# Kernel optimization log

Measured on AMD Instinct MI355X. Metric: run time of the kernel, lower is better.

The kernel has to match this reference:

```python
import jax, jax.numpy as jnp
import numpy as np

EMBED_DIM = 1024
N_HEADS = 16
HEAD_DIM = EMBED_DIM // N_HEADS


def setup_inputs() -> dict:
    key = jax.random.key(0)
    k_x, k_qw, k_qb, k_ow, k_ob = jax.random.split(key, 5)
    s = 1.0 / np.sqrt(EMBED_DIM)
    return {
        "x": jax.random.normal(k_x, (2, 2048, EMBED_DIM), dtype=jnp.float32),
        "qkv_w": jax.random.uniform(k_qw, (3 * EMBED_DIM, EMBED_DIM), jnp.float32, -s, s),
        "qkv_b": jax.random.uniform(k_qb, (3 * EMBED_DIM,), jnp.float32, -s, s),
        "out_w": jax.random.uniform(k_ow, (EMBED_DIM, EMBED_DIM), jnp.float32, -s, s),
        "out_b": jax.random.uniform(k_ob, (EMBED_DIM,), jnp.float32, -s, s),
    }


def reference(x, qkv_w, qkv_b, out_w, out_b):
    B, S, E = x.shape
    # fused QKV projection (torch Linear: x @ W^T + b)
    qkv = x @ qkv_w.T + qkv_b                      # [B,S,3E]
    qkv = qkv.reshape(B, S, N_HEADS, 3 * HEAD_DIM).transpose(0, 2, 1, 3)  # [B,H,S,3d]
    q, k, v = jnp.split(qkv, 3, axis=-1)           # each [B,H,S,d]
    scores = jnp.einsum("bhqd,bhkd->bhqk", q, k) / jnp.sqrt(jnp.float32(HEAD_DIM))
    weights = jax.nn.softmax(scores, axis=-1)      # [B,H,S,S]
    attn = jnp.einsum("bhqk,bhkd->bhqd", weights, v)
    attn = attn.transpose(0, 2, 1, 3).reshape(B, S, E)
    return attn @ out_w.T + out_b
```

## Files before the change

kernel.cpp:

```cpp
#include <hip/hip_runtime.h>
#include <hip/hip_bf16.h>


#define E_DIM   1024
#define NHEADS  16
#define HDIM    64
#define SEQ     2048
#define TOK     4096
#define QKV_DIM 3072
#define QK_STRIDE 2048
#define QSCALE_F 0.18033688011112042f

typedef __attribute__((ext_vector_type(8))) short bf16x8;
typedef __attribute__((ext_vector_type(4))) float f32x4;
typedef __attribute__((ext_vector_type(4))) int   i32x4;
typedef __attribute__((ext_vector_type(2))) int   i32x2;
typedef __attribute__((ext_vector_type(2))) __bf16 bf16x2_t;

#if __has_builtin(__builtin_amdgcn_exp2f)
#define EXP2F(x) __builtin_amdgcn_exp2f(x)
#else
#define EXP2F(x) exp2f(x)
#endif

__device__ __forceinline__ unsigned pack2bf(float a, float b) {
#if __has_builtin(__builtin_amdgcn_cvt_pk_bf16_f32)
    union { bf16x2_t v; unsigned u; } u;
    u.v = __builtin_amdgcn_cvt_pk_bf16_f32(a, b);
    return u.u;
#else
    union { float f; unsigned u; } ua, ub; ua.f = a; ub.f = b;
    unsigned ra = ua.u + 0x7FFF + ((ua.u >> 16) & 1);
    unsigned rb = ub.u + 0x7FFF + ((ub.u >> 16) & 1);
    return (ra >> 16) | (rb & 0xFFFF0000u);
#endif
}

__device__ __forceinline__ unsigned short f2bf(float x) {
    return (unsigned short)(pack2bf(x, x) & 0xFFFFu);
}

__device__ __forceinline__ void load_lds16(const void* g, void* l) {
    __builtin_amdgcn_global_load_lds(
        (const __attribute__((address_space(1))) void*)g,
        (__attribute__((address_space(3))) void*)l, 16, 0, 0);
}

__device__ __forceinline__ bf16x8 lds_read8(const unsigned short* p) {
    union { i32x4 i; bf16x8 b; } u;
    u.i = *(const i32x4*)p;
    return u.b;
}

__device__ __forceinline__ f32x4 mfma16(bf16x8 a, bf16x8 b, f32x4 c) {
    return __builtin_amdgcn_mfma_f32_16x16x32_bf16(a, b, c, 0, 0, 0);
}

__global__ void cast3_kernel(const float* __restrict__ a, unsigned short* __restrict__ oa, int na4,
                             const float* __restrict__ b, unsigned short* __restrict__ ob, int nb4,
                             const float* __restrict__ c, unsigned short* __restrict__ oc) {
    int i = blockIdx.x * blockDim.x + threadIdx.x;
    const float* src; unsigned short* dst; int j;
    if (i < na4)            { src = a; dst = oa; j = i; }
    else if (i < na4 + nb4) { src = b; dst = ob; j = i - na4; }
    else                    { src = c; dst = oc; j = i - na4 - nb4; }
    f32x4 v = ((const f32x4*)src)[j];
    union { i32x2 i2; unsigned u[2]; } o;
    o.u[0] = pack2bf(v.x, v.y);
    o.u[1] = pack2bf(v.z, v.w);
    ((i32x2*)dst)[j] = o.i2;
}

__global__ __launch_bounds__(256, 3)
void gemm_qkv_kernel(const unsigned short* __restrict__ A,
                     const unsigned short* __restrict__ B,
                     const float* __restrict__ bias,
                     unsigned short* __restrict__ qk,
                     unsigned short* __restrict__ vT,
                     int K) {
    __shared__ __align__(16) unsigned short As[128 * 64];
    __shared__ __align__(16) unsigned short Bs[128 * 64];

    const int tid  = threadIdx.x;
    const int wave = tid >> 6, lane = tid & 63;
    const int quad = lane >> 4, l16 = lane & 15;
    const int flat = blockIdx.y * 24 + blockIdx.x;
    const int xcd = flat & 7, idx = flat >> 3;
    const int row_blk = (xcd >> 1) * 8 + idx / 12;
    const int col_blk = (xcd & 1) * 12 + idx % 12;
    const int row0 = row_blk * 128, col0 = col_blk * 128;
    const int wr = (wave >> 1) * 64, wc = (wave & 1) * 64;

    f32x4 acc[4][4];
#pragma unroll
    for (int i = 0; i < 4; ++i)
#pragma unroll
        for (int j = 0; j < 4; ++j) acc[i][j] = (f32x4){0.f, 0.f, 0.f, 0.f};

    const int nkt = K >> 6;
    for (int kt = 0; kt < nkt; ++kt) {
        const int k0 = kt << 6;
#pragma unroll
        for (int i = 0; i < 4; ++i) {
            int p = i * 256 + tid;
            int r = p >> 3;
            int kc = (p & 7) ^ (r & 7);
            load_lds16(A + (size_t)(row0 + r) * K + k0 + kc * 8, &As[p * 8]);
        }
#pragma unroll
        for (int i = 0; i < 4; ++i) {
            int p = i * 256 + tid;
            int r = p >> 3;
            int kc = (p & 7) ^ (r & 7);
            load_lds16(B + (size_t)(col0 + r) * K + k0 + kc * 8, &Bs[p * 8]);
        }
        __syncthreads();

#pragma unroll
        for (int ks = 0; ks < 2; ++ks) {
            bf16x8 af[4], bfr[4];
#pragma unroll
            for (int rb = 0; rb < 4; ++rb) {
                int r_l  = wr + rb * 16 + l16;
                int phys = (ks * 4 + quad) ^ (l16 & 7);
                af[rb] = lds_read8(&As[r_l * 64 + phys * 8]);
            }
#pragma unroll
            for (int cb = 0; cb < 4; ++cb) {
                int r_l  = wc + cb * 16 + l16;
                int phys = (ks * 4 + quad) ^ (l16 & 7);
                bfr[cb] = lds_read8(&Bs[r_l * 64 + phys * 8]);
            }
#pragma unroll
            for (int rb = 0; rb < 4; ++rb)
#pragma unroll
                for (int cb = 0; cb < 4; ++cb)
                    acc[rb][cb] = mfma16(af[rb], bfr[cb], acc[rb][cb]);
        }
        __syncthreads();
    }

#pragma unroll
    for (int rb = 0; rb < 4; ++rb)
#pragma unroll
        for (int cb = 0; cb < 4; ++cb) {
            int col = col0 + wc + cb * 16 + l16;
            int h    = col / 192;
            int part = col - h * 192;
            float bv = bias[col];
            int row_b = row0 + wr + rb * 16 + quad * 4;
            float v[4];
#pragma unroll
            for (int reg = 0; reg < 4; ++reg) v[reg] = acc[rb][cb][reg] + bv;
            if (part < 128) {
                float sc = (part < 64) ? QSCALE_F : 1.0f;
                size_t base = (size_t)h * 128 + part;
#pragma unroll
                for (int reg = 0; reg < 4; ++reg)
                    qk[(size_t)(row_b + reg) * QK_STRIDE + base] = f2bf(v[reg] * sc);
            } else {
                int i  = part - 128;
                int b  = row_b >> 11;
                int s0 = row_b & 2047;
                int kk = s0 & 127;
                int cc = kk >> 4, qq = (kk >> 2) & 3;
                int sp = (s0 & ~127) | ((cc >> 1) << 5) | (qq << 3) | ((cc & 1) << 2);
                i32x2 pk;
                pk.x = (int)pack2bf(v[0], v[1]);
                pk.y = (int)pack2bf(v[2], v[3]);
                *(i32x2*)&vT[(((size_t)(b * 16 + h)) * 64 + i) * SEQ + sp] = pk;
            }
        }
}

__global__ __launch_bounds__(256, 2)
void gemm2_kernel(const unsigned short* __restrict__ A,
                  const unsigned short* __restrict__ B,
                  const float* __restrict__ bias,
                  float* __restrict__ C, int M, int N, int K) {
    __shared__ __align__(16) unsigned short As[128 * 64];
    __shared__ __align__(16) unsigned short Bs[64 * 64];

    const int tid  = threadIdx.x;
    const int wave = tid >> 6, lane = tid & 63;
    const int quad = lane >> 4, l16 = lane & 15;
    const int flat = blockIdx.y * 16 + blockIdx.x;
    const int xcd = flat & 7, idx = flat >> 3;
    const int row_blk = (xcd >> 1) * 8 + (idx >> 3);
    const int col_blk = (xcd & 1) * 8 + (idx & 7);
    const int row0 = row_blk * 128, col0 = col_blk * 64;
    const int wr = wave * 32;

    f32x4 acc[2][4];
#pragma unroll
    for (int i = 0; i < 2; ++i)
#pragma unroll
        for (int j = 0; j < 4; ++j) acc[i][j] = (f32x4){0.f, 0.f, 0.f, 0.f};

    const int nkt = K >> 6;
    for (int kt = 0; kt < nkt; ++kt) {
        const int k0 = kt << 6;
#pragma unroll
        for (int i = 0; i < 4; ++i) {
            int p = i * 256 + tid;
            int r = p >> 3;
            int kc = (p & 7) ^ (r & 7);
            load_lds16(A + (size_t)(row0 + r) * K + k0 + kc * 8, &As[p * 8]);
        }
#pragma unroll
        for (int i = 0; i < 2; ++i) {
            int p = i * 256 + tid;
            int r = p >> 3;
            int kc = (p & 7) ^ (r & 7);
            load_lds16(B + (size_t)(col0 + r) * K + k0 + kc * 8, &Bs[p * 8]);
        }
        __syncthreads();

#pragma unroll
        for (int ks = 0; ks < 2; ++ks) {
            bf16x8 af[2], bfr[4];
#pragma unroll
            for (int rb = 0; rb < 2; ++rb) {
                int r_l  = wr + rb * 16 + l16;
                int phys = (ks * 4 + quad) ^ (l16 & 7);
                af[rb] = lds_read8(&As[r_l * 64 + phys * 8]);
            }
#pragma unroll
            for (int cb = 0; cb < 4; ++cb) {
                int r_l  = cb * 16 + l16;
                int phys = (ks * 4 + quad) ^ (l16 & 7);
                bfr[cb] = lds_read8(&Bs[r_l * 64 + phys * 8]);
            }
#pragma unroll
            for (int rb = 0; rb < 2; ++rb)
#pragma unroll
                for (int cb = 0; cb < 4; ++cb)
                    acc[rb][cb] = mfma16(af[rb], bfr[cb], acc[rb][cb]);
        }
        __syncthreads();
    }

#pragma unroll
    for (int rb = 0; rb < 2; ++rb)
#pragma unroll
        for (int cb = 0; cb < 4; ++cb) {
            int col = col0 + cb * 16 + l16;
            float bv = bias[col];
#pragma unroll
            for (int reg = 0; reg < 4; ++reg) {
                int row = row0 + wr + rb * 16 + quad * 4 + reg;
                C[(size_t)row * N + col] = acc[rb][cb][reg] + bv;
            }
        }
}


#define STAGE_KV(BUF) do {                                                     \
    load_lds16(kg[0], lk[0] + (BUF) * 8192); kg[0] += 128 * QK_STRIDE;         \
    load_lds16(kg[1], lk[1] + (BUF) * 8192); kg[1] += 128 * QK_STRIDE;         \
    load_lds16(vg[0], lv[0] + (BUF) * 8192); vg[0] += 128;                     \
    load_lds16(vg[1], lv[1] + (BUF) * 8192); vg[1] += 128;                     \
} while (0)

#define COMPUTE_TILE(BUF) do {                                                 \
    constexpr int KO_ = (BUF) * 8192;                                          \
    f32x4 s[8];                                                                \
    _Pragma("unroll") for (int cb = 0; cb < 8; ++cb)                           \
        s[cb] = (f32x4){0.f, 0.f, 0.f, 0.f};                                   \
    __builtin_amdgcn_s_setprio(1);                                             \
    _Pragma("unroll") for (int cb = 0; cb < 8; ++cb) {                         \
        bf16x8 kf0 = lds_read8(Kb0 + KO_ + cb * 1024);                         \
        s[cb] = mfma16(kf0, qf[0], s[cb]);                                     \
    }                                                                          \
    _Pragma("unroll") for (int cb = 0; cb < 8; ++cb) {                         \
        bf16x8 kf1 = lds_read8(Kb1 + KO_ + cb * 1024);                         \
        s[cb] = mfma16(kf1, qf[1], s[cb]);                                     \
    }                                                                          \
    __builtin_amdgcn_s_setprio(0);                                             \
    _Pragma("unroll") for (int cb = 0; cb < 8; ++cb)                           \
        _Pragma("unroll") for (int r = 0; r < 4; ++r)                          \
            s[cb][r] = EXP2F(s[cb][r]);                                        \
    {                                                                          \
        f32x4 t0 = s[0] + s[1], t1 = s[2] + s[3];                              \
        f32x4 t2 = s[4] + s[5], t3 = s[6] + s[7];                              \
        t0 += t1; t2 += t3;                                                    \
        lsum += t0 + t2;                                                       \
    }                                                                          \
    __builtin_amdgcn_s_setprio(1);                                             \
    _Pragma("unroll") for (int ks2 = 0; ks2 < 4; ++ks2) {                      \
        union { i32x4 i; bf16x8 b; } pu;                                       \
        pu.i.x = (int)pack2bf(s[2 * ks2][0], s[2 * ks2][1]);                   \
        pu.i.y = (int)pack2bf(s[2 * ks2][2], s[2 * ks2][3]);                   \
        pu.i.z = (int)pack2bf(s[2 * ks2 + 1][0], s[2 * ks2 + 1][1]);           \
        pu.i.w = (int)pack2bf(s[2 * ks2 + 1][2], s[2 * ks2 + 1][3]);           \
        bf16x8 pf = pu.b;                                                      \
        _Pragma("unroll") for (int ib = 0; ib < 4; ++ib) {                     \
            bf16x8 vf = lds_read8(Vb[ks2] + KO_ + ib * 2048);                  \
            o[ib] = mfma16(pf, vf, o[ib]);                                     \
        }                                                                      \
    }                                                                          \
    __builtin_amdgcn_s_setprio(0);                                             \
} while (0)

__global__ __launch_bounds__(512, 4)
void attn_kernel(const unsigned short* __restrict__ qk,
                 const unsigned short* __restrict__ vT,
                 unsigned short* __restrict__ attn) {
    __shared__ __align__(16) unsigned short Ks[2][128 * 64];
    __shared__ __align__(16) unsigned short Vs[2][64 * 128];

    const int tid  = threadIdx.x;
    const int wave = tid >> 6, lane = tid & 63;
    const int quad = lane >> 4, l16 = lane & 15;

    const int flat = blockIdx.y * 16 + blockIdx.x;
    const int swz  = (flat & 7) * 64 + (flat >> 3);
    const int bh = swz >> 4;
    const int b = bh >> 4, h = bh & 15;
    const int q0 = (swz & 15) * 128;
    const size_t rowbase = (size_t)b * SEQ;
    const int qtok = q0 + wave * 16 + l16;

    const int sw3 = l16 & 7;
    const unsigned short* Kb0 = &Ks[0][l16 * 64 + ((quad ^ sw3) * 8)];
    const unsigned short* Kb1 = &Ks[0][l16 * 64 + (((4 + quad) ^ sw3) * 8)];
    const unsigned short* Vb[4] = {
        &Vs[0][l16 * 128 + (((0 * 4 + quad) ^ l16) * 8)],
        &Vs[0][l16 * 128 + (((1 * 4 + quad) ^ l16) * 8)],
        &Vs[0][l16 * 128 + (((2 * 4 + quad) ^ l16) * 8)],
        &Vs[0][l16 * 128 + (((3 * 4 + quad) ^ l16) * 8)] };

    const unsigned short* kg[2]; unsigned short* lk[2];
    const unsigned short* vg[2]; unsigned short* lv[2];
#pragma unroll
    for (int i = 0; i < 2; ++i) {
        int p = i * 512 + tid;
        { int r = p >> 3; int kc = (p & 7) ^ (r & 7);
          kg[i] = qk + (rowbase) * QK_STRIDE + h * 128 + 64 + (size_t)r * QK_STRIDE + kc * 8;
          lk[i] = &Ks[0][p * 8]; }
        { int r = p >> 4; int c = (p & 15) ^ (r & 15);
          vg[i] = vT + (size_t)bh * 64 * SEQ + (size_t)r * SEQ + c * 8;
          lv[i] = &Vs[0][p * 8]; }
    }

    bf16x8 qf[2];
#pragma unroll
    for (int ks = 0; ks < 2; ++ks) {
        const unsigned short* p =
            qk + (rowbase + qtok) * QK_STRIDE + h * 128 + ks * 32 + quad * 8;
        union { i32x4 i; bf16x8 b; } u;
        u.i = *(const i32x4*)p;
        qf[ks] = u.b;
    }

    f32x4 o[4];
#pragma unroll
    for (int ib = 0; ib < 4; ++ib) o[ib] = (f32x4){0.f, 0.f, 0.f, 0.f};
    f32x4 lsum = (f32x4){0.f, 0.f, 0.f, 0.f};

    STAGE_KV(0);
#pragma unroll 1
    for (int kt = 0; kt < SEQ / 128; kt += 2) {
        STAGE_KV(1);
        __asm__ volatile("s_waitcnt vmcnt(4)" ::: "memory");
        __builtin_amdgcn_s_barrier();
        COMPUTE_TILE(0);
        __builtin_amdgcn_s_barrier();
        if (kt + 2 < SEQ / 128) {
            STAGE_KV(0);
            __asm__ volatile("s_waitcnt vmcnt(4)" ::: "memory");
        } else {
            __asm__ volatile("s_waitcnt vmcnt(0)" ::: "memory");
        }
        __builtin_amdgcn_s_barrier();
        COMPUTE_TILE(1);
        __builtin_amdgcn_s_barrier();
    }

    float l_p = (lsum[0] + lsum[1]) + (lsum[2] + lsum[3]);
    l_p += __shfl_xor(l_p, 16);
    l_p += __shfl_xor(l_p, 32);

    float il[4];
#pragma unroll
    for (int r = 0; r < 4; ++r) il[r] = 1.0f / __shfl(l_p, quad * 4 + r);
#pragma unroll
    for (int ib = 0; ib < 4; ++ib)
#pragma unroll
        for (int r = 0; r < 4; ++r) {
            int t = q0 + wave * 16 + quad * 4 + r;
            attn[(rowbase + t) * E_DIM + h * 64 + ib * 16 + l16] =
                f2bf(o[ib][r] * il[r]);
        }
}

extern "C" void kernel_launch(void* const* d_in, const int* in_sizes, int n_in,
                              void* d_out, int out_size, void* d_ws, size_t ws_size,
                              hipStream_t stream) {
    const float* x     = (const float*)d_in[0];
    const float* qkv_w = (const float*)d_in[1];
    const float* qkv_b = (const float*)d_in[2];
    const float* out_w = (const float*)d_in[3];
    const float* out_b = (const float*)d_in[4];

    char* ws = (char*)d_ws;
    unsigned short* xb   = (unsigned short*)(ws);
    unsigned short* wqkv = (unsigned short*)(ws + 8388608);
    unsigned short* wout = (unsigned short*)(ws + 14680064);
    unsigned short* qk   = (unsigned short*)(ws + 16777216);
    unsigned short* attn = (unsigned short*)(ws + 33554432);
    unsigned short* vT   = (unsigned short*)(ws + 41943040);

    cast3_kernel<<<8192, 256, 0, stream>>>(x, xb, 1048576,
                                           qkv_w, wqkv, 786432,
                                           out_w, wout);

    gemm_qkv_kernel<<<dim3(24, 32), 256, 0, stream>>>(
        xb, wqkv, qkv_b, qk, vT, E_DIM);

    attn_kernel<<<dim3(16, 32), 512, 0, stream>>>(qk, vT, attn);

    gemm2_kernel<<<dim3(16, 32), 256, 0, stream>>>(
        attn, wout, out_b, (float*)d_out, TOK, E_DIM, E_DIM);
}
```

Before: 174.8 us.

## Double-buffer LDS staging in QKV and output-projection GEMMs

Both GEMM kernels now use two LDS buffers and issue the global-to-LDS loads for the next K tile before computing the current one, using explicit vmcnt waits and raw barriers. Global load latency can then overlap MFMA work instead of being exposed each iteration. It doubles LDS use (the QKV kernel drops from 3 to 2 blocks per CU) and hardcodes 16 K-tiles, so K must equal 1024.

```diff
diff --git a/kernel.cpp b/kernel.cpp
--- a/kernel.cpp
+++ b/kernel.cpp
@@ -71,15 +71,45 @@
     ((i32x2*)dst)[j] = o.i2;
 }
 
-__global__ __launch_bounds__(256, 3)
+
+#define STAGE_G1(BUF) do {                                                     \
+    _Pragma("unroll") for (int i_ = 0; i_ < 4; ++i_) {                         \
+        load_lds16(ag[i_], la[i_] + (BUF) * 8192); ag[i_] += 64;               \
+    }                                                                          \
+    _Pragma("unroll") for (int i_ = 0; i_ < 4; ++i_) {                         \
+        load_lds16(bg[i_], lb[i_] + (BUF) * 8192); bg[i_] += 64;               \
+    }                                                                          \
+} while (0)
+
+#define COMP_G1(BUF) do {                                                      \
+    constexpr int KO_ = (BUF) * 8192;                                          \
+    _Pragma("unroll") for (int ks = 0; ks < 2; ++ks) {                         \
+        bf16x8 af[4], bfr[4];                                                  \
+        _Pragma("unroll") for (int rb = 0; rb < 4; ++rb) {                     \
+            int r_l  = wr + rb * 16 + l16;                                     \
+            int phys = (ks * 4 + quad) ^ (l16 & 7);                            \
+            af[rb] = lds_read8(&As[0][KO_ + r_l * 64 + phys * 8]);             \
+        }                                                                      \
+        _Pragma("unroll") for (int cb = 0; cb < 4; ++cb) {                     \
+            int r_l  = wc + cb * 16 + l16;                                     \
+            int phys = (ks * 4 + quad) ^ (l16 & 7);                            \
+            bfr[cb] = lds_read8(&Bs[0][KO_ + r_l * 64 + phys * 8]);            \
+        }                                                                      \
+        _Pragma("unroll") for (int rb = 0; rb < 4; ++rb)                       \
+            _Pragma("unroll") for (int cb = 0; cb < 4; ++cb)                   \
+                acc[rb][cb] = mfma16(af[rb], bfr[cb], acc[rb][cb]);            \
+    }                                                                          \
+} while (0)
+
+__global__ __launch_bounds__(256, 2)
 void gemm_qkv_kernel(const unsigned short* __restrict__ A,
                      const unsigned short* __restrict__ B,
                      const float* __restrict__ bias,
                      unsigned short* __restrict__ qk,
                      unsigned short* __restrict__ vT,
                      int K) {
-    __shared__ __align__(16) unsigned short As[128 * 64];
-    __shared__ __align__(16) unsigned short Bs[128 * 64];
+    __shared__ __align__(16) unsigned short As[2][128 * 64];
+    __shared__ __align__(16) unsigned short Bs[2][128 * 64];
 
     const int tid  = threadIdx.x;
     const int wave = tid >> 6, lane = tid & 63;
@@ -91,53 +121,42 @@
     const int row0 = row_blk * 128, col0 = col_blk * 128;
     const int wr = (wave >> 1) * 64, wc = (wave & 1) * 64;
 
+    const unsigned short* ag[4]; unsigned short* la[4];
+    const unsigned short* bg[4]; unsigned short* lb[4];
+#pragma unroll
+    for (int i = 0; i < 4; ++i) {
+        int p = i * 256 + tid;
+        int r = p >> 3;
+        int kc = (p & 7) ^ (r & 7);
+        ag[i] = A + (size_t)(row0 + r) * K + kc * 8;
+        la[i] = &As[0][p * 8];
+        bg[i] = B + (size_t)(col0 + r) * K + kc * 8;
+        lb[i] = &Bs[0][p * 8];
+    }
+
     f32x4 acc[4][4];
 #pragma unroll
     for (int i = 0; i < 4; ++i)
 #pragma unroll
         for (int j = 0; j < 4; ++j) acc[i][j] = (f32x4){0.f, 0.f, 0.f, 0.f};
 
-    const int nkt = K >> 6;
-    for (int kt = 0; kt < nkt; ++kt) {
-        const int k0 = kt << 6;
-#pragma unroll
-        for (int i = 0; i < 4; ++i) {
-            int p = i * 256 + tid;
-            int r = p >> 3;
-            int kc = (p & 7) ^ (r & 7);
-            load_lds16(A + (size_t)(row0 + r) * K + k0 + kc * 8, &As[p * 8]);
-        }
-#pragma unroll
-        for (int i = 0; i < 4; ++i) {
-            int p = i * 256 + tid;
-            int r = p >> 3;
-            int kc = (p & 7) ^ (r & 7);
-            load_lds16(B + (size_t)(col0 + r) * K + k0 + kc * 8, &Bs[p * 8]);
-        }
-        __syncthreads();
-
-#pragma unroll
-        for (int ks = 0; ks < 2; ++ks) {
-            bf16x8 af[4], bfr[4];
-#pragma unroll
-            for (int rb = 0; rb < 4; ++rb) {
-                int r_l  = wr + rb * 16 + l16;
-                int phys = (ks * 4 + quad) ^ (l16 & 7);
-                af[rb] = lds_read8(&As[r_l * 64 + phys * 8]);
-            }
-#pragma unroll
-            for (int cb = 0; cb < 4; ++cb) {
-                int r_l  = wc + cb * 16 + l16;
-                int phys = (ks * 4 + quad) ^ (l16 & 7);
-                bfr[cb] = lds_read8(&Bs[r_l * 64 + phys * 8]);
-            }
-#pragma unroll
-            for (int rb = 0; rb < 4; ++rb)
-#pragma unroll
-                for (int cb = 0; cb < 4; ++cb)
-                    acc[rb][cb] = mfma16(af[rb], bfr[cb], acc[rb][cb]);
-        }
-        __syncthreads();
+    STAGE_G1(0);
+#pragma unroll 1
+    for (int kt = 0; kt < 16; kt += 2) {
+        STAGE_G1(1);
+        __asm__ volatile("s_waitcnt vmcnt(8)" ::: "memory");
+        __builtin_amdgcn_s_barrier();
+        COMP_G1(0);
+        __builtin_amdgcn_s_barrier();
+        if (kt + 2 < 16) {
+            STAGE_G1(0);
+            __asm__ volatile("s_waitcnt vmcnt(8)" ::: "memory");
+        } else {
+            __asm__ volatile("s_waitcnt vmcnt(0)" ::: "memory");
+        }
+        __builtin_amdgcn_s_barrier();
+        COMP_G1(1);
+        __builtin_amdgcn_s_barrier();
     }
 
 #pragma unroll
@@ -173,13 +192,44 @@
         }
 }
 
+
+#define STAGE_G2(BUF) do {                                                     \
+    _Pragma("unroll") for (int i_ = 0; i_ < 4; ++i_) {                         \
+        load_lds16(ag[i_], la[i_] + (BUF) * 8192); ag[i_] += 64;               \
+    }                                                                          \
+    _Pragma("unroll") for (int i_ = 0; i_ < 2; ++i_) {                         \
+        load_lds16(bg[i_], lb[i_] + (BUF) * 4096); bg[i_] += 64;               \
+    }                                                                          \
+} while (0)
+
+#define COMP_G2(BUF) do {                                                      \
+    constexpr int AO_ = (BUF) * 8192;                                          \
+    constexpr int BO_ = (BUF) * 4096;                                          \
+    _Pragma("unroll") for (int ks = 0; ks < 2; ++ks) {                         \
+        bf16x8 af[2], bfr[4];                                                  \
+        _Pragma("unroll") for (int rb = 0; rb < 2; ++rb) {                     \
+            int r_l  = wr + rb * 16 + l16;                                     \
+            int phys = (ks * 4 + quad) ^ (l16 & 7);                            \
+            af[rb] = lds_read8(&As[0][AO_ + r_l * 64 + phys * 8]);             \
+        }                                                                      \
+        _Pragma("unroll") for (int cb = 0; cb < 4; ++cb) {                     \
+            int r_l  = cb * 16 + l16;                                          \
+            int phys = (ks * 4 + quad) ^ (l16 & 7);                            \
+            bfr[cb] = lds_read8(&Bs[0][BO_ + r_l * 64 + phys * 8]);            \
+        }                                                                      \
+        _Pragma("unroll") for (int rb = 0; rb < 2; ++rb)                       \
+            _Pragma("unroll") for (int cb = 0; cb < 4; ++cb)                   \
+                acc[rb][cb] = mfma16(af[rb], bfr[cb], acc[rb][cb]);            \
+    }                                                                          \
+} while (0)
+
 __global__ __launch_bounds__(256, 2)
 void gemm2_kernel(const unsigned short* __restrict__ A,
                   const unsigned short* __restrict__ B,
                   const float* __restrict__ bias,
                   float* __restrict__ C, int M, int N, int K) {
-    __shared__ __align__(16) unsigned short As[128 * 64];
-    __shared__ __align__(16) unsigned short Bs[64 * 64];
+    __shared__ __align__(16) unsigned short As[2][128 * 64];
+    __shared__ __align__(16) unsigned short Bs[2][64 * 64];
 
     const int tid  = threadIdx.x;
     const int wave = tid >> 6, lane = tid & 63;
@@ -191,53 +241,48 @@
     const int row0 = row_blk * 128, col0 = col_blk * 64;
     const int wr = wave * 32;
 
+    const unsigned short* ag[4]; unsigned short* la[4];
+    const unsigned short* bg[2]; unsigned short* lb[2];
+#pragma unroll
+    for (int i = 0; i < 4; ++i) {
+        int p = i * 256 + tid;
+        int r = p >> 3;
+        int kc = (p & 7) ^ (r & 7);
+        ag[i] = A + (size_t)(row0 + r) * K + kc * 8;
+        la[i] = &As[0][p * 8];
+    }
+#pragma unroll
+    for (int i = 0; i < 2; ++i) {
+        int p = i * 256 + tid;
+        int r = p >> 3;
+        int kc = (p & 7) ^ (r & 7);
+        bg[i] = B + (size_t)(col0 + r) * K + kc * 8;
+        lb[i] = &Bs[0][p * 8];
+    }
+
     f32x4 acc[2][4];
 #pragma unroll
     for (int i = 0; i < 2; ++i)
 #pragma unroll
         for (int j = 0; j < 4; ++j) acc[i][j] = (f32x4){0.f, 0.f, 0.f, 0.f};
 
-    const int nkt = K >> 6;
-    for (int kt = 0; kt < nkt; ++kt) {
-        const int k0 = kt << 6;
-#pragma unroll
-        for (int i = 0; i < 4; ++i) {
-            int p = i * 256 + tid;
-            int r = p >> 3;
-            int kc = (p & 7) ^ (r & 7);
-            load_lds16(A + (size_t)(row0 + r) * K + k0 + kc * 8, &As[p * 8]);
-        }
-#pragma unroll
-        for (int i = 0; i < 2; ++i) {
-            int p = i * 256 + tid;
-            int r = p >> 3;
-            int kc = (p & 7) ^ (r & 7);
-            load_lds16(B + (size_t)(col0 + r) * K + k0 + kc * 8, &Bs[p * 8]);
-        }
-        __syncthreads();
-
-#pragma unroll
-        for (int ks = 0; ks < 2; ++ks) {
-            bf16x8 af[2], bfr[4];
-#pragma unroll
-            for (int rb = 0; rb < 2; ++rb) {
-                int r_l  = wr + rb * 16 + l16;
-                int phys = (ks * 4 + quad) ^ (l16 & 7);
-                af[rb] = lds_read8(&As[r_l * 64 + phys * 8]);
-            }
-#pragma unroll
-            for (int cb = 0; cb < 4; ++cb) {
-                int r_l  = cb * 16 + l16;
-                int phys = (ks * 4 + quad) ^ (l16 & 7);
-                bfr[cb] = lds_read8(&Bs[r_l * 64 + phys * 8]);
-            }
-#pragma unroll
-            for (int rb = 0; rb < 2; ++rb)
-#pragma unroll
-                for (int cb = 0; cb < 4; ++cb)
-                    acc[rb][cb] = mfma16(af[rb], bfr[cb], acc[rb][cb]);
-        }
-        __syncthreads();
+    STAGE_G2(0);
+#pragma unroll 1
+    for (int kt = 0; kt < 16; kt += 2) {
+        STAGE_G2(1);
+        __asm__ volatile("s_waitcnt vmcnt(6)" ::: "memory");
+        __builtin_amdgcn_s_barrier();
+        COMP_G2(0);
+        __builtin_amdgcn_s_barrier();
+        if (kt + 2 < 16) {
+            STAGE_G2(0);
+            __asm__ volatile("s_waitcnt vmcnt(6)" ::: "memory");
+        } else {
+            __asm__ volatile("s_waitcnt vmcnt(0)" ::: "memory");
+        }
+        __builtin_amdgcn_s_barrier();
+        COMP_G2(1);
+        __builtin_amdgcn_s_barrier();
     }
 
 #pragma unroll
```

Result: slower. 178.7 us (+2.3%).

## Software-pipeline attention loop so QK of next tile overlaps softmax-PV of previous

Applied to the files above, without the earlier changes.

Splits the per-tile compute into a QK^T stage and an exp/PV stage, and splits KV staging into separate K and V loads. The main loop now issues QK for the current tile together with softmax and PV for the previous tile, using two score register sets, with a prologue and epilogue. The aim is to interleave MFMA work with exp/transcendental work and shorten the dependency stalls between the two matmuls. The second score array raises register pressure under launch_bounds(512,4), and the hand-tuned vmcnt waits plus buffer reuse add a risk of LDS races.

```diff
diff --git a/kernel.cpp b/kernel.cpp
--- a/kernel.cpp
+++ b/kernel.cpp
@@ -255,44 +255,49 @@
 }
 
 
-#define STAGE_KV(BUF) do {                                                     \
+#define STAGE_K(BUF) do {                                                      \
     load_lds16(kg[0], lk[0] + (BUF) * 8192); kg[0] += 128 * QK_STRIDE;         \
     load_lds16(kg[1], lk[1] + (BUF) * 8192); kg[1] += 128 * QK_STRIDE;         \
+} while (0)
+#define STAGE_V(BUF) do {                                                      \
     load_lds16(vg[0], lv[0] + (BUF) * 8192); vg[0] += 128;                     \
     load_lds16(vg[1], lv[1] + (BUF) * 8192); vg[1] += 128;                     \
 } while (0)
 
-#define COMPUTE_TILE(BUF) do {                                                 \
+#define QK_TILE(S, BUF) do {                                                   \
     constexpr int KO_ = (BUF) * 8192;                                          \
-    f32x4 s[8];                                                                \
     _Pragma("unroll") for (int cb = 0; cb < 8; ++cb)                           \
-        s[cb] = (f32x4){0.f, 0.f, 0.f, 0.f};                                   \
+        S[cb] = (f32x4){0.f, 0.f, 0.f, 0.f};                                   \
     __builtin_amdgcn_s_setprio(1);                                             \
     _Pragma("unroll") for (int cb = 0; cb < 8; ++cb) {                         \
         bf16x8 kf0 = lds_read8(Kb0 + KO_ + cb * 1024);                         \
-        s[cb] = mfma16(kf0, qf[0], s[cb]);                                     \
+        S[cb] = mfma16(kf0, qf[0], S[cb]);                                     \
     }                                                                          \
     _Pragma("unroll") for (int cb = 0; cb < 8; ++cb) {                         \
         bf16x8 kf1 = lds_read8(Kb1 + KO_ + cb * 1024);                         \
-        s[cb] = mfma16(kf1, qf[1], s[cb]);                                     \
+        S[cb] = mfma16(kf1, qf[1], S[cb]);                                     \
     }                                                                          \
     __builtin_amdgcn_s_setprio(0);                                             \
+} while (0)
+
+#define SMPV_TILE(S, BUF) do {                                                 \
+    constexpr int KO_ = (BUF) * 8192;                                          \
     _Pragma("unroll") for (int cb = 0; cb < 8; ++cb)                           \
         _Pragma("unroll") for (int r = 0; r < 4; ++r)                          \
-            s[cb][r] = EXP2F(s[cb][r]);                                        \
+            S[cb][r] = EXP2F(S[cb][r]);                                        \
     {                                                                          \
-        f32x4 t0 = s[0] + s[1], t1 = s[2] + s[3];                              \
-        f32x4 t2 = s[4] + s[5], t3 = s[6] + s[7];                              \
+        f32x4 t0 = S[0] + S[1], t1 = S[2] + S[3];                              \
+        f32x4 t2 = S[4] + S[5], t3 = S[6] + S[7];                              \
         t0 += t1; t2 += t3;                                                    \
         lsum += t0 + t2;                                                       \
     }                                                                          \
     __builtin_amdgcn_s_setprio(1);                                             \
     _Pragma("unroll") for (int ks2 = 0; ks2 < 4; ++ks2) {                      \
         union { i32x4 i; bf16x8 b; } pu;                                       \
-        pu.i.x = (int)pack2bf(s[2 * ks2][0], s[2 * ks2][1]);                   \
-        pu.i.y = (int)pack2bf(s[2 * ks2][2], s[2 * ks2][3]);                   \
-        pu.i.z = (int)pack2bf(s[2 * ks2 + 1][0], s[2 * ks2 + 1][1]);           \
-        pu.i.w = (int)pack2bf(s[2 * ks2 + 1][2], s[2 * ks2 + 1][3]);           \
+        pu.i.x = (int)pack2bf(S[2 * ks2][0], S[2 * ks2][1]);                   \
+        pu.i.y = (int)pack2bf(S[2 * ks2][2], S[2 * ks2][3]);                   \
+        pu.i.z = (int)pack2bf(S[2 * ks2 + 1][0], S[2 * ks2 + 1][1]);           \
+        pu.i.w = (int)pack2bf(S[2 * ks2 + 1][2], S[2 * ks2 + 1][3]);           \
         bf16x8 pf = pu.b;                                                      \
         _Pragma("unroll") for (int ib = 0; ib < 4; ++ib) {                     \
             bf16x8 vf = lds_read8(Vb[ks2] + KO_ + ib * 2048);                  \
@@ -300,6 +305,16 @@
         }                                                                      \
     }                                                                          \
     __builtin_amdgcn_s_setprio(0);                                             \
+} while (0)
+
+#define ATTN_ITER(SC, SP, CUR) do {                                            \
+    __asm__ volatile("s_waitcnt vmcnt(2)" ::: "memory");                       \
+    __builtin_amdgcn_s_barrier();                                              \
+    QK_TILE(SC, CUR);                                                          \
+    SMPV_TILE(SP, (CUR) ^ 1);                                                  \
+    __builtin_amdgcn_s_barrier();                                              \
+    STAGE_K((CUR) ^ 1);                                                        \
+    STAGE_V((CUR) ^ 1);                                                        \
 } while (0)
 
 __global__ __launch_bounds__(512, 4)
@@ -358,24 +373,27 @@
     for (int ib = 0; ib < 4; ++ib) o[ib] = (f32x4){0.f, 0.f, 0.f, 0.f};
     f32x4 lsum = (f32x4){0.f, 0.f, 0.f, 0.f};
 
-    STAGE_KV(0);
+    f32x4 sA[8], sB[8];
+
+    STAGE_K(0); STAGE_V(0);
+    STAGE_K(1); STAGE_V(1);
+    __asm__ volatile("s_waitcnt vmcnt(4)" ::: "memory");
+    __builtin_amdgcn_s_barrier();
+    QK_TILE(sA, 0);
+
 #pragma unroll 1
-    for (int kt = 0; kt < SEQ / 128; kt += 2) {
-        STAGE_KV(1);
-        __asm__ volatile("s_waitcnt vmcnt(4)" ::: "memory");
-        __builtin_amdgcn_s_barrier();
-        COMPUTE_TILE(0);
-        __builtin_amdgcn_s_barrier();
-        if (kt + 2 < SEQ / 128) {
-            STAGE_KV(0);
-            __asm__ volatile("s_waitcnt vmcnt(4)" ::: "memory");
-        } else {
-            __asm__ volatile("s_waitcnt vmcnt(0)" ::: "memory");
-        }
-        __builtin_amdgcn_s_barrier();
-        COMPUTE_TILE(1);
-        __builtin_amdgcn_s_barrier();
+    for (int kt = 1; kt < 15; kt += 2) {
+        ATTN_ITER(sB, sA, 1);
+        ATTN_ITER(sA, sB, 0);
     }
+
+    __asm__ volatile("s_waitcnt vmcnt(2)" ::: "memory");
+    __builtin_amdgcn_s_barrier();
+    QK_TILE(sB, 1);
+    SMPV_TILE(sA, 0);
+    __asm__ volatile("s_waitcnt vmcnt(0)" ::: "memory");
+    __builtin_amdgcn_s_barrier();
+    SMPV_TILE(sB, 1);
 
     float l_p = (lsum[0] + lsum[1]) + (lsum[2] + lsum[3]);
     l_p += __shfl_xor(l_p, 16);
```

After: 198.1 us. 13.3% more time.

## Single-buffer V in LDS and split K/V waits to raise attention occupancy

Applied to the files above, without the earlier changes.

The attention kernel now keeps K double-buffered but uses a single LDS buffer for V, staging each V tile after the PV matmul. It waits for K before QK^T and for V only before PV, with extra barriers. Launch bounds go from 4 to 6 blocks per CU. The aim is to cut LDS use so more blocks can be resident to hide latency. In exchange there are more barriers per tile and less prefetch distance on V, which could expose load latency.

```diff
diff --git a/kernel.cpp b/kernel.cpp
--- a/kernel.cpp
+++ b/kernel.cpp
@@ -255,15 +255,19 @@
 }
 
 
-#define STAGE_KV(BUF) do {                                                     \
-    load_lds16(kg[0], lk[0] + (BUF) * 8192); kg[0] += 128 * QK_STRIDE;         \
-    load_lds16(kg[1], lk[1] + (BUF) * 8192); kg[1] += 128 * QK_STRIDE;         \
-    load_lds16(vg[0], lv[0] + (BUF) * 8192); vg[0] += 128;                     \
-    load_lds16(vg[1], lv[1] + (BUF) * 8192); vg[1] += 128;                     \
+#define STAGE_K3(P) do {                                                       \
+    load_lds16(kg[0], lk[0] + (P) * 8192); kg[0] += 128 * QK_STRIDE;           \
+    load_lds16(kg[1], lk[1] + (P) * 8192); kg[1] += 128 * QK_STRIDE;           \
 } while (0)
-
-#define COMPUTE_TILE(BUF) do {                                                 \
-    constexpr int KO_ = (BUF) * 8192;                                          \
+#define STAGE_V3() do {                                                        \
+    load_lds16(vg[0], lv[0]); vg[0] += 128;                                    \
+    load_lds16(vg[1], lv[1]); vg[1] += 128;                                    \
+} while (0)
+
+#define ATTN_ITER3(P, KW, VW, DO_V, DO_K) do {                                 \
+    __asm__ volatile("s_waitcnt vmcnt(" #KW ")" ::: "memory");                 \
+    __builtin_amdgcn_s_barrier();                                              \
+    constexpr int KO_ = (P) * 8192;                                            \
     f32x4 s[8];                                                                \
     _Pragma("unroll") for (int cb = 0; cb < 8; ++cb)                           \
         s[cb] = (f32x4){0.f, 0.f, 0.f, 0.f};                                   \
@@ -286,6 +290,8 @@
         t0 += t1; t2 += t3;                                                    \
         lsum += t0 + t2;                                                       \
     }                                                                          \
+    __asm__ volatile("s_waitcnt vmcnt(" #VW ")" ::: "memory");                 \
+    __builtin_amdgcn_s_barrier();                                              \
     __builtin_amdgcn_s_setprio(1);                                             \
     _Pragma("unroll") for (int ks2 = 0; ks2 < 4; ++ks2) {                      \
         union { i32x4 i; bf16x8 b; } pu;                                       \
@@ -295,19 +301,22 @@
         pu.i.w = (int)pack2bf(s[2 * ks2 + 1][2], s[2 * ks2 + 1][3]);           \
         bf16x8 pf = pu.b;                                                      \
         _Pragma("unroll") for (int ib = 0; ib < 4; ++ib) {                     \
-            bf16x8 vf = lds_read8(Vb[ks2] + KO_ + ib * 2048);                  \
+            bf16x8 vf = lds_read8(Vb[ks2] + ib * 2048);                        \
             o[ib] = mfma16(pf, vf, o[ib]);                                     \
         }                                                                      \
     }                                                                          \
     __builtin_amdgcn_s_setprio(0);                                             \
+    __builtin_amdgcn_s_barrier();                                              \
+    if (DO_V) STAGE_V3();                                                      \
+    if (DO_K) STAGE_K3(P);                                                     \
 } while (0)
 
-__global__ __launch_bounds__(512, 4)
+__global__ __launch_bounds__(512, 6)
 void attn_kernel(const unsigned short* __restrict__ qk,
                  const unsigned short* __restrict__ vT,
                  unsigned short* __restrict__ attn) {
     __shared__ __align__(16) unsigned short Ks[2][128 * 64];
-    __shared__ __align__(16) unsigned short Vs[2][64 * 128];
+    __shared__ __align__(16) unsigned short Vs[64 * 128];
 
     const int tid  = threadIdx.x;
     const int wave = tid >> 6, lane = tid & 63;
@@ -325,10 +334,10 @@
     const unsigned short* Kb0 = &Ks[0][l16 * 64 + ((quad ^ sw3) * 8)];
     const unsigned short* Kb1 = &Ks[0][l16 * 64 + (((4 + quad) ^ sw3) * 8)];
     const unsigned short* Vb[4] = {
-        &Vs[0][l16 * 128 + (((0 * 4 + quad) ^ l16) * 8)],
-        &Vs[0][l16 * 128 + (((1 * 4 + quad) ^ l16) * 8)],
-        &Vs[0][l16 * 128 + (((2 * 4 + quad) ^ l16) * 8)],
-        &Vs[0][l16 * 128 + (((3 * 4 + quad) ^ l16) * 8)] };
+        &Vs[l16 * 128 + (((0 * 4 + quad) ^ l16) * 8)],
+        &Vs[l16 * 128 + (((1 * 4 + quad) ^ l16) * 8)],
+        &Vs[l16 * 128 + (((2 * 4 + quad) ^ l16) * 8)],
+        &Vs[l16 * 128 + (((3 * 4 + quad) ^ l16) * 8)] };
 
     const unsigned short* kg[2]; unsigned short* lk[2];
     const unsigned short* vg[2]; unsigned short* lv[2];
@@ -340,7 +349,7 @@
           lk[i] = &Ks[0][p * 8]; }
         { int r = p >> 4; int c = (p & 15) ^ (r & 15);
           vg[i] = vT + (size_t)bh * 64 * SEQ + (size_t)r * SEQ + c * 8;
-          lv[i] = &Vs[0][p * 8]; }
+          lv[i] = &Vs[p * 8]; }
     }
 
     bf16x8 qf[2];
@@ -358,24 +367,17 @@
     for (int ib = 0; ib < 4; ++ib) o[ib] = (f32x4){0.f, 0.f, 0.f, 0.f};
     f32x4 lsum = (f32x4){0.f, 0.f, 0.f, 0.f};
 
-    STAGE_KV(0);
+    STAGE_K3(0);
+    STAGE_V3();
+    STAGE_K3(1);
+
 #pragma unroll 1
-    for (int kt = 0; kt < SEQ / 128; kt += 2) {
-        STAGE_KV(1);
-        __asm__ volatile("s_waitcnt vmcnt(4)" ::: "memory");
-        __builtin_amdgcn_s_barrier();
-        COMPUTE_TILE(0);
-        __builtin_amdgcn_s_barrier();
-        if (kt + 2 < SEQ / 128) {
-            STAGE_KV(0);
-            __asm__ volatile("s_waitcnt vmcnt(4)" ::: "memory");
-        } else {
-            __asm__ volatile("s_waitcnt vmcnt(0)" ::: "memory");
-        }
-        __builtin_amdgcn_s_barrier();
-        COMPUTE_TILE(1);
-        __builtin_amdgcn_s_barrier();
+    for (int kt = 0; kt < 14; kt += 2) {
+        ATTN_ITER3(0, 4, 2, 1, 1);
+        ATTN_ITER3(1, 4, 2, 1, 1);
     }
+    ATTN_ITER3(0, 4, 2, 1, 0);
+    ATTN_ITER3(1, 2, 0, 0, 0);
 
     float l_p = (lsum[0] + lsum[1]) + (lsum[2] + lsum[3]);
     l_p += __shfl_xor(l_p, 16);
```

New measurement: 220.4 us. 26.1% more time.
